# Performance work log

Hardware: AMD Instinct MI355X
Metric: run time of the kernel (lower is better)

Reference implementation:

```python
import jax, jax.numpy as jnp
import numpy as np

B, S, N, E = 8, 64, 512, 32  # batch, seq_size, node_num, embed_size


def setup_inputs() -> dict:
    key = jax.random.key(0)
    k0, k1, k2, k3, k4 = jax.random.split(key, 5)
    x = jax.random.normal(k0, (B, S, N), dtype=jnp.float32)
    # lin_w: Linear(2*S, E) -> weight (E, 2*S), bias (E,)
    W = jax.random.normal(k1, (E, 2 * S), dtype=jnp.float32) * (1.0 / np.sqrt(2 * S))
    b_w = jax.random.normal(k2, (E,), dtype=jnp.float32) * 0.01
    # lin_a: Linear(E, 1) -> weight (E,), bias scalar
    Wa = jax.random.normal(k3, (E,), dtype=jnp.float32) * (1.0 / np.sqrt(E))
    b_a = jax.random.normal(k4, (), dtype=jnp.float32) * 0.01
    return {"x": x, "W": W, "b_w": b_w, "Wa": Wa, "b_a": b_a}


def reference(x, W, b_w, Wa, b_a):
    # Faithful to MP_GAT.forward in eval mode (dropout = identity).
    # Algebraic decomposition: lin_w(cat(vi, vj)) = vi @ Wi^T + vj @ Wj^T + b,
    # where W = [Wi | Wj] along the input dim -- avoids the O(N^2 * 2S) concat.
    s = W.shape[1] // 2
    v = jnp.transpose(x, (0, 2, 1))          # (B, N, S)
    Wi, Wj = W[:, :s], W[:, s:]              # (E, S) each
    ti = jnp.einsum('bns,es->bne', v, Wi)    # (B, N, E)
    tj = jnp.einsum('bns,es->bne', v, Wj)    # (B, N, E)
    pre = ti[:, :, None, :] + tj[:, None, :, :] + b_w  # (B, N, N, E)
    xw = jnp.where(pre > 0, pre, 0.2 * pre)  # LeakyReLU(0.2)
    e = jnp.einsum('bije,e->bij', xw, Wa) + b_a        # (B, N, N) = lin_a(...).squeeze
    attention = jax.nn.softmax(e, axis=2)
    h = jax.nn.sigmoid(jnp.einsum('bij,bjs->bis', attention, v))  # (B, N, S)
    return jnp.transpose(h, (0, 2, 1)), attention      # (B, S, N), (B, N, N)
```

## Files before the change

### kernel.cpp

```cpp
#include <hip/hip_runtime.h>
#include <math.h>

#define BB 8
#define SS 64
#define NN 512
#define EE 32
#define IT 16

__device__ __forceinline__ int swz(int i, int j) {
    return (((i >> 2) ^ ((j >> 3) & 3)) << 2) | (i & 3);
}

__global__ __launch_bounds__(256) void proj_kernel(
    const float* __restrict__ x, const float* __restrict__ W,
    const float* __restrict__ b_w, const float* __restrict__ Wa,
    float* __restrict__ tip, float* __restrict__ tjp,
    float* __restrict__ cip, float* __restrict__ djp)
{
    __shared__ float sW[SS][65];
    const int t = threadIdx.x;
    const int b = blockIdx.x >> 5;
    const int n0 = (blockIdx.x & 31) << 4;

#pragma unroll
    for (int r = 0; r < 4; ++r) {
        int idx = r * 1024 + t * 4;
        float4 w4 = *(const float4*)(W + idx);
        int e = idx >> 7;
        int sp = idx & 127;
        int eo = ((sp >> 6) << 5) | e;
        int s0 = sp & 63;
        sW[s0 + 0][eo] = w4.x;
        sW[s0 + 1][eo] = w4.y;
        sW[s0 + 2][eo] = w4.z;
        sW[s0 + 3][eo] = w4.w;
    }
    __syncthreads();

    const int eo = t & 63;
    const int ng = t >> 6;
    const float* xb = x + (size_t)b * SS * NN + n0 + (ng << 2);
    float a0 = 0.f, a1 = 0.f, a2 = 0.f, a3 = 0.f;
#pragma unroll 8
    for (int s = 0; s < SS; ++s) {
        float wv = sW[s][eo];
        float4 xv = *(const float4*)(xb + (size_t)s * NN);
        a0 = fmaf(wv, xv.x, a0);
        a1 = fmaf(wv, xv.y, a1);
        a2 = fmaf(wv, xv.z, a2);
        a3 = fmaf(wv, xv.w, a3);
    }
    const int e = eo & 31;
    const bool isI = eo < EE;
    float bias = isI ? b_w[e] : 0.f;
    a0 += bias; a1 += bias; a2 += bias; a3 += bias;
    float* dst = isI ? tip : tjp;
    *(float4*)(dst + ((size_t)(b * EE + e)) * NN + n0 + (ng << 2)) =
        make_float4(a0, a1, a2, a3);

    float wa = Wa[e];
    float r0 = wa * a0, r1 = wa * a1, r2 = wa * a2, r3 = wa * a3;
#pragma unroll
    for (int off = 1; off <= 16; off <<= 1) {
        r0 += __shfl_xor(r0, off);
        r1 += __shfl_xor(r1, off);
        r2 += __shfl_xor(r2, off);
        r3 += __shfl_xor(r3, off);
    }
    if (eo == 0)
        *(float4*)(cip + (size_t)b * NN + n0 + (ng << 2)) = make_float4(r0, r1, r2, r3);
    if (eo == 32)
        *(float4*)(djp + (size_t)b * NN + n0 + (ng << 2)) = make_float4(r0, r1, r2, r3);
}

__global__ __launch_bounds__(512, 2) void attn_kernel(
    const float* __restrict__ x,
    const float* __restrict__ tip,
    const float* __restrict__ tjp,
    const float* __restrict__ cip,
    const float* __restrict__ djp,
    const float* __restrict__ Wa,
    float* __restrict__ out0,
    float* __restrict__ out1)
{
    __shared__ float s_tiT[IT][36];
    __shared__ float scT[NN][20];
    __shared__ float red1[8][17];
    __shared__ float s_M[IT];
    __shared__ float s_inv[IT];
    __shared__ __align__(16) float ubuf[EE * NN];

    float (*stj)[NN] = (float (*)[NN])ubuf;

    const int t = threadIdx.x;
    const int b = blockIdx.x >> 5;
    const int i0 = (blockIdx.x & 31) << 4;

    {
        int e = t >> 4, ii = t & 15;
        s_tiT[ii][e] = tip[((size_t)(b * EE + e)) * NN + i0 + ii];
    }
    {
        const float4* src = (const float4*)(tjp + (size_t)b * EE * NN);
        float4* dst4 = (float4*)ubuf;
#pragma unroll
        for (int r = 0; r < 8; ++r) dst4[r * 512 + t] = src[r * 512 + t];
    }
    __syncthreads();

    const int ip = t & 7;
    const int jc = t >> 3;
    const int jb0 = jc << 3;
    const int ia = 2 * ip, ibb = 2 * ip + 1;

    float rti0[EE], rti1[EE];
#pragma unroll
    for (int q = 0; q < 8; ++q) {
        float4 v = *(const float4*)(&s_tiT[ia][q << 2]);
        rti0[4 * q + 0] = v.x; rti0[4 * q + 1] = v.y;
        rti0[4 * q + 2] = v.z; rti0[4 * q + 3] = v.w;
        float4 w = *(const float4*)(&s_tiT[ibb][q << 2]);
        rti1[4 * q + 0] = w.x; rti1[4 * q + 1] = w.y;
        rti1[4 * q + 2] = w.z; rti1[4 * q + 3] = w.w;
    }

    float acc0[8], acc1[8];
#pragma unroll
    for (int k = 0; k < 8; ++k) { acc0[k] = 0.f; acc1[k] = 0.f; }

#pragma unroll
    for (int e = 0; e < EE; ++e) {
        float wa = Wa[e];
        float t0 = rti0[e], t1 = rti1[e];
        float4 ja = *(const float4*)(&stj[e][jb0]);
        float4 jb = *(const float4*)(&stj[e][jb0 + 4]);
        float tj8[8] = {ja.x, ja.y, ja.z, ja.w, jb.x, jb.y, jb.z, jb.w};
#pragma unroll
        for (int k = 0; k < 8; ++k) {
            float p0 = fmaxf(t0 + tj8[k], 0.f);
            acc0[k] = fmaf(p0, wa, acc0[k]);
            float p1 = fmaxf(t1 + tj8[k], 0.f);
            acc1[k] = fmaf(p1, wa, acc1[k]);
        }
    }

    float dj8[8];
    {
        float4 d0 = *(const float4*)(djp + (size_t)b * NN + jb0);
        float4 d1 = *(const float4*)(djp + (size_t)b * NN + jb0 + 4);
        dj8[0] = d0.x; dj8[1] = d0.y; dj8[2] = d0.z; dj8[3] = d0.w;
        dj8[4] = d1.x; dj8[5] = d1.y; dj8[6] = d1.z; dj8[7] = d1.w;
    }
    float c0 = 0.2f * cip[(size_t)b * NN + i0 + ia];
    float c1 = 0.2f * cip[(size_t)b * NN + i0 + ibb];
    float sc0[8], sc1[8];
#pragma unroll
    for (int k = 0; k < 8; ++k) {
        sc0[k] = fmaf(0.8f, acc0[k], fmaf(0.2f, dj8[k], c0));
        sc1[k] = fmaf(0.8f, acc1[k], fmaf(0.2f, dj8[k], c1));
    }

    float m0 = sc0[0], m1 = sc1[0];
#pragma unroll
    for (int k = 1; k < 8; ++k) { m0 = fmaxf(m0, sc0[k]); m1 = fmaxf(m1, sc1[k]); }
#pragma unroll
    for (int off = 8; off <= 32; off <<= 1) {
        m0 = fmaxf(m0, __shfl_xor(m0, off));
        m1 = fmaxf(m1, __shfl_xor(m1, off));
    }
    const int wv = t >> 6;
    if ((t & 56) == 0) { red1[wv][ia] = m0; red1[wv][ibb] = m1; }
    __syncthreads();
    if (t < IT) {
        float M = red1[0][t];
#pragma unroll
        for (int g = 1; g < 8; ++g) M = fmaxf(M, red1[g][t]);
        s_M[t] = M;
    }
    __syncthreads();

    float M0 = s_M[ia], M1 = s_M[ibb];
    float pr0[8], pr1[8];
#pragma unroll
    for (int k = 0; k < 8; ++k) {
        pr0[k] = __expf(sc0[k] - M0);
        pr1[k] = __expf(sc1[k] - M1);
    }
#pragma unroll
    for (int k = 0; k < 8; ++k) {
        int j = jb0 + k;
        scT[j][swz(ia, j)] = pr0[k];
        scT[j][swz(ibb, j)] = pr1[k];
    }
    float q0 = 0.f, q1 = 0.f;
#pragma unroll
    for (int k = 0; k < 8; ++k) { q0 += pr0[k]; q1 += pr1[k]; }
#pragma unroll
    for (int off = 8; off <= 32; off <<= 1) {
        q0 += __shfl_xor(q0, off);
        q1 += __shfl_xor(q1, off);
    }
    if ((t & 56) == 0) { red1[wv][ia] = q0; red1[wv][ibb] = q1; }
    __syncthreads();
    if (t < IT) {
        float S = 0.f;
#pragma unroll
        for (int g = 0; g < 8; ++g) S += red1[g][t];
        s_inv[t] = 1.0f / S;
    }
    __syncthreads();

    {
        float v0 = s_inv[ia], v1 = s_inv[ibb];
        float* r0p = out1 + ((size_t)(b * NN + i0 + ia)) * NN + jb0;
        float* r1p = out1 + ((size_t)(b * NN + i0 + ibb)) * NN + jb0;
        *(float4*)(r0p)     = make_float4(pr0[0]*v0, pr0[1]*v0, pr0[2]*v0, pr0[3]*v0);
        *(float4*)(r0p + 4) = make_float4(pr0[4]*v0, pr0[5]*v0, pr0[6]*v0, pr0[7]*v0);
        *(float4*)(r1p)     = make_float4(pr1[0]*v1, pr1[1]*v1, pr1[2]*v1, pr1[3]*v1);
        *(float4*)(r1p + 4) = make_float4(pr1[4]*v1, pr1[5]*v1, pr1[6]*v1, pr1[7]*v1);
    }

    const int jw = t & 3, sq = (t >> 2) & 7, ih = (t >> 5) & 1, w8 = t >> 6;
    float pacc[8][8];
#pragma unroll
    for (int r = 0; r < 8; ++r)
#pragma unroll
        for (int c = 0; c < 8; ++c) pacc[r][c] = 0.f;

    const float* xbb = x + (size_t)b * SS * NN;
#pragma unroll
    for (int uu = 0; uu < 4; ++uu) {
        const int jb = uu * 128 + w8 * 16 + jw * 4;
        float xq[8][4];
#pragma unroll
        for (int r = 0; r < 8; ++r) {
            float4 xv = *(const float4*)(xbb + (size_t)(sq + 8 * r) * NN + jb);
            xq[r][0] = xv.x; xq[r][1] = xv.y; xq[r][2] = xv.z; xq[r][3] = xv.w;
        }
#pragma unroll
        for (int v = 0; v < 4; ++v) {
            int j2 = jb + v;
            int key = (j2 >> 3) & 3;
            float4 pA4 = *(const float4*)(&scT[j2][((2 * ih) ^ key) << 2]);
            float4 pB4 = *(const float4*)(&scT[j2][((2 * ih + 1) ^ key) << 2]);
            float pA[4] = {pA4.x, pA4.y, pA4.z, pA4.w};
            float pB[4] = {pB4.x, pB4.y, pB4.z, pB4.w};
#pragma unroll
            for (int r = 0; r < 8; ++r) {
                float xv = xq[r][v];
#pragma unroll
                for (int c = 0; c < 4; ++c) {
                    pacc[r][c]     = fmaf(xv, pA[c], pacc[r][c]);
                    pacc[r][4 + c] = fmaf(xv, pB[c], pacc[r][4 + c]);
                }
            }
        }
    }

#pragma unroll
    for (int r = 0; r < 8; ++r)
#pragma unroll
        for (int c = 0; c < 8; ++c) {
            float v = pacc[r][c];
            v += __int_as_float(__builtin_amdgcn_mov_dpp(__float_as_int(v), 0xB1, 0xF, 0xF, true));
            v += __int_as_float(__builtin_amdgcn_mov_dpp(__float_as_int(v), 0x4E, 0xF, 0xF, true));
            pacc[r][c] = v;
        }
    if (jw == 0) {
#pragma unroll
        for (int r = 0; r < 8; ++r) {
            int s = sq + 8 * r;
            float* hq = &ubuf[(size_t)(w8 * SS + s) * 20 + ih * 8];
            *(float4*)(hq)     = make_float4(pacc[r][0], pacc[r][1], pacc[r][2], pacc[r][3]);
            *(float4*)(hq + 4) = make_float4(pacc[r][4], pacc[r][5], pacc[r][6], pacc[r][7]);
        }
    }
    __syncthreads();

    {
        int i = t & 15, sp = t >> 4;
        float vi = s_inv[i];
#pragma unroll
        for (int p = 0; p < 2; ++p) {
            int s = sp + 32 * p;
            float h = 0.f;
#pragma unroll
            for (int wq = 0; wq < 8; ++wq) h += ubuf[(size_t)(wq * SS + s) * 20 + i];
            h *= vi;
            out0[((size_t)(b * SS + s)) * NN + i0 + i] = 1.0f / (1.0f + __expf(-h));
        }
    }
}

extern "C" void kernel_launch(void* const* d_in, const int* in_sizes, int n_in,
                              void* d_out, int out_size, void* d_ws, size_t ws_size,
                              hipStream_t stream) {
    const float* x   = (const float*)d_in[0];
    const float* W   = (const float*)d_in[1];
    const float* b_w = (const float*)d_in[2];
    const float* Wa  = (const float*)d_in[3];

    float* out0 = (float*)d_out;
    float* out1 = (float*)d_out + (size_t)BB * SS * NN;

    float* tip = (float*)d_ws;
    float* tjp = tip + (size_t)BB * EE * NN;
    float* cip = tjp + (size_t)BB * EE * NN;
    float* djp = cip + (size_t)BB * NN;

    proj_kernel<<<BB * (NN / 16), 256, 0, stream>>>(x, W, b_w, Wa, tip, tjp, cip, djp);
    attn_kernel<<<BB * (NN / IT), 512, 0, stream>>>(x, tip, tjp, cip, djp, Wa, out0, out1);
}
```

Measured before the change: 23.59 us.

## Store tj and softmax probabilities as bf16, drop max pass, use abs LeakyReLU form

The tj projection is written to the workspace as packed bf16, halving the global and shared traffic for the tj tile in the attention kernel. Unnormalized probabilities are also kept in LDS as packed bf16, and the PV loop unpacks eight values from a single 16-byte read. LeakyReLU is rewritten as 0.6x + 0.4|x|, which folds the linear part into the precomputed ci/dj terms. The softmax max-reduction pass and its two barriers are removed, and block indices are remapped across XCDs with a smaller proj block. The risks are bf16 rounding error in the attention weights and exp overflow when scores are large, since the max is no longer subtracted.

After: 22.22 us. 5.8% less time.

```diff
diff --git a/kernel.cpp b/kernel.cpp
--- a/kernel.cpp
+++ b/kernel.cpp
@@ -7,24 +7,35 @@
 #define EE 32
 #define IT 16
 
-__device__ __forceinline__ int swz(int i, int j) {
-    return (((i >> 2) ^ ((j >> 3) & 3)) << 2) | (i & 3);
-}
-
-__global__ __launch_bounds__(256) void proj_kernel(
+__device__ __forceinline__ unsigned short f2bf(float f) {
+    union { float f; unsigned u; } v; v.f = f;
+    unsigned r = v.u + 0x7fffu + ((v.u >> 16) & 1u);
+    return (unsigned short)(r >> 16);
+}
+__device__ __forceinline__ float bflo(unsigned u) { return __uint_as_float(u << 16); }
+__device__ __forceinline__ float bfhi(unsigned u) { return __uint_as_float(u & 0xffff0000u); }
+
+__device__ __forceinline__ float qsum(float v) {
+    v += __int_as_float(__builtin_amdgcn_mov_dpp(__float_as_int(v), 0xB1, 0xF, 0xF, true));
+    v += __int_as_float(__builtin_amdgcn_mov_dpp(__float_as_int(v), 0x4E, 0xF, 0xF, true));
+    return v;
+}
+
+__global__ __launch_bounds__(128) void proj_kernel(
     const float* __restrict__ x, const float* __restrict__ W,
     const float* __restrict__ b_w, const float* __restrict__ Wa,
-    float* __restrict__ tip, float* __restrict__ tjp,
+    float* __restrict__ tip, unsigned short* __restrict__ tjb,
     float* __restrict__ cip, float* __restrict__ djp)
 {
     __shared__ float sW[SS][65];
     const int t = threadIdx.x;
-    const int b = blockIdx.x >> 5;
-    const int n0 = (blockIdx.x & 31) << 4;
-
-#pragma unroll
-    for (int r = 0; r < 4; ++r) {
-        int idx = r * 1024 + t * 4;
+    const int wg = ((blockIdx.x & 7) << 6) | (blockIdx.x >> 3);
+    const int b = wg >> 6;
+    const int n0 = (wg & 63) << 3;
+
+#pragma unroll
+    for (int r = 0; r < 8; ++r) {
+        int idx = r * 512 + t * 4;
         float4 w4 = *(const float4*)(W + idx);
         int e = idx >> 7;
         int sp = idx & 127;
@@ -52,11 +63,17 @@
     }
     const int e = eo & 31;
     const bool isI = eo < EE;
-    float bias = isI ? b_w[e] : 0.f;
-    a0 += bias; a1 += bias; a2 += bias; a3 += bias;
-    float* dst = isI ? tip : tjp;
-    *(float4*)(dst + ((size_t)(b * EE + e)) * NN + n0 + (ng << 2)) =
-        make_float4(a0, a1, a2, a3);
+    if (isI) {
+        float bias = b_w[e];
+        a0 += bias; a1 += bias; a2 += bias; a3 += bias;
+        *(float4*)(tip + ((size_t)(b * EE + e)) * NN + n0 + (ng << 2)) =
+            make_float4(a0, a1, a2, a3);
+    } else {
+        unsigned u0 = f2bf(a0) | ((unsigned)f2bf(a1) << 16);
+        unsigned u1 = f2bf(a2) | ((unsigned)f2bf(a3) << 16);
+        *(uint2*)(tjb + ((size_t)(b * EE + e)) * NN + n0 + (ng << 2)) =
+            make_uint2(u0, u1);
+    }
 
     float wa = Wa[e];
     float r0 = wa * a0, r1 = wa * a1, r2 = wa * a2, r3 = wa * a3;
@@ -76,52 +93,53 @@
 __global__ __launch_bounds__(512, 2) void attn_kernel(
     const float* __restrict__ x,
     const float* __restrict__ tip,
-    const float* __restrict__ tjp,
+    const unsigned short* __restrict__ tjb,
     const float* __restrict__ cip,
     const float* __restrict__ djp,
     const float* __restrict__ Wa,
     float* __restrict__ out0,
     float* __restrict__ out1)
 {
-    __shared__ float s_tiT[IT][36];
-    __shared__ float scT[NN][20];
-    __shared__ float red1[8][17];
-    __shared__ float s_M[IT];
+    __shared__ __align__(16) unsigned short stj[EE * NN];
+    __shared__ __align__(16) unsigned scT[NN * 12];
+    __shared__ __align__(16) float s_tiT[IT][36];
+    __shared__ __align__(16) float hp[8 * SS * 20];
+    __shared__ __align__(16) float red[8][IT];
     __shared__ float s_inv[IT];
-    __shared__ __align__(16) float ubuf[EE * NN];
-
-    float (*stj)[NN] = (float (*)[NN])ubuf;
 
     const int t = threadIdx.x;
-    const int b = blockIdx.x >> 5;
-    const int i0 = (blockIdx.x & 31) << 4;
-
-    {
-        int e = t >> 4, ii = t & 15;
-        s_tiT[ii][e] = tip[((size_t)(b * EE + e)) * NN + i0 + ii];
-    }
-    {
-        const float4* src = (const float4*)(tjp + (size_t)b * EE * NN);
-        float4* dst4 = (float4*)ubuf;
-#pragma unroll
-        for (int r = 0; r < 8; ++r) dst4[r * 512 + t] = src[r * 512 + t];
+    const int wg = ((blockIdx.x & 7) << 5) | (blockIdx.x >> 3);
+    const int b = wg >> 5;
+    const int i0 = (wg & 31) << 4;
+    const int lane = t & 63;
+    const int w = t >> 6;
+
+    {
+        int i = t & 15, e = t >> 4;
+        s_tiT[i][e] = tip[((size_t)(b * EE + e)) * NN + i0 + i];
+    }
+    {
+        const uint4* src = (const uint4*)(tjb + (size_t)b * EE * NN);
+        uint4* dst = (uint4*)stj;
+#pragma unroll
+        for (int r = 0; r < 4; ++r) dst[r * 512 + t] = src[r * 512 + t];
     }
     __syncthreads();
 
     const int ip = t & 7;
     const int jc = t >> 3;
-    const int jb0 = jc << 3;
-    const int ia = 2 * ip, ibb = 2 * ip + 1;
+    const int j0 = jc << 3;
+    const int ia = 2 * ip, ib2 = 2 * ip + 1;
 
     float rti0[EE], rti1[EE];
 #pragma unroll
     for (int q = 0; q < 8; ++q) {
-        float4 v = *(const float4*)(&s_tiT[ia][q << 2]);
+        float4 v = *(const float4*)&s_tiT[ia][q << 2];
         rti0[4 * q + 0] = v.x; rti0[4 * q + 1] = v.y;
         rti0[4 * q + 2] = v.z; rti0[4 * q + 3] = v.w;
-        float4 w = *(const float4*)(&s_tiT[ibb][q << 2]);
-        rti1[4 * q + 0] = w.x; rti1[4 * q + 1] = w.y;
-        rti1[4 * q + 2] = w.z; rti1[4 * q + 3] = w.w;
+        float4 u = *(const float4*)&s_tiT[ib2][q << 2];
+        rti1[4 * q + 0] = u.x; rti1[4 * q + 1] = u.y;
+        rti1[4 * q + 2] = u.z; rti1[4 * q + 3] = u.w;
     }
 
     float acc0[8], acc1[8];
@@ -130,97 +148,74 @@
 
 #pragma unroll
     for (int e = 0; e < EE; ++e) {
+        uint4 d = *(const uint4*)&stj[e * NN + j0];
         float wa = Wa[e];
         float t0 = rti0[e], t1 = rti1[e];
-        float4 ja = *(const float4*)(&stj[e][jb0]);
-        float4 jb = *(const float4*)(&stj[e][jb0 + 4]);
-        float tj8[8] = {ja.x, ja.y, ja.z, ja.w, jb.x, jb.y, jb.z, jb.w};
+        float tjf[8];
+        tjf[0] = bflo(d.x); tjf[1] = bfhi(d.x);
+        tjf[2] = bflo(d.y); tjf[3] = bfhi(d.y);
+        tjf[4] = bflo(d.z); tjf[5] = bfhi(d.z);
+        tjf[6] = bflo(d.w); tjf[7] = bfhi(d.w);
 #pragma unroll
         for (int k = 0; k < 8; ++k) {
-            float p0 = fmaxf(t0 + tj8[k], 0.f);
-            acc0[k] = fmaf(p0, wa, acc0[k]);
-            float p1 = fmaxf(t1 + tj8[k], 0.f);
-            acc1[k] = fmaf(p1, wa, acc1[k]);
+            acc0[k] = fmaf(fabsf(t0 + tjf[k]), wa, acc0[k]);
+            acc1[k] = fmaf(fabsf(t1 + tjf[k]), wa, acc1[k]);
         }
     }
 
     float dj8[8];
     {
-        float4 d0 = *(const float4*)(djp + (size_t)b * NN + jb0);
-        float4 d1 = *(const float4*)(djp + (size_t)b * NN + jb0 + 4);
+        float4 d0 = *(const float4*)(djp + (size_t)b * NN + j0);
+        float4 d1 = *(const float4*)(djp + (size_t)b * NN + j0 + 4);
         dj8[0] = d0.x; dj8[1] = d0.y; dj8[2] = d0.z; dj8[3] = d0.w;
         dj8[4] = d1.x; dj8[5] = d1.y; dj8[6] = d1.z; dj8[7] = d1.w;
     }
-    float c0 = 0.2f * cip[(size_t)b * NN + i0 + ia];
-    float c1 = 0.2f * cip[(size_t)b * NN + i0 + ibb];
-    float sc0[8], sc1[8];
+    float c0 = cip[(size_t)b * NN + i0 + ia];
+    float c1 = cip[(size_t)b * NN + i0 + ib2];
+    float pr0[8], pr1[8];
 #pragma unroll
     for (int k = 0; k < 8; ++k) {
-        sc0[k] = fmaf(0.8f, acc0[k], fmaf(0.2f, dj8[k], c0));
-        sc1[k] = fmaf(0.8f, acc1[k], fmaf(0.2f, dj8[k], c1));
-    }
-
-    float m0 = sc0[0], m1 = sc1[0];
-#pragma unroll
-    for (int k = 1; k < 8; ++k) { m0 = fmaxf(m0, sc0[k]); m1 = fmaxf(m1, sc1[k]); }
+        pr0[k] = __expf(fmaf(0.4f, acc0[k], 0.6f * (c0 + dj8[k])));
+        pr1[k] = __expf(fmaf(0.4f, acc1[k], 0.6f * (c1 + dj8[k])));
+    }
+
+#pragma unroll
+    for (int k = 0; k < 8; ++k) {
+        scT[(j0 + k) * 12 + ip] = f2bf(pr0[k]) | ((unsigned)f2bf(pr1[k]) << 16);
+    }
+
+    float rs0 = 0.f, rs1 = 0.f;
+#pragma unroll
+    for (int k = 0; k < 8; ++k) { rs0 += pr0[k]; rs1 += pr1[k]; }
 #pragma unroll
     for (int off = 8; off <= 32; off <<= 1) {
-        m0 = fmaxf(m0, __shfl_xor(m0, off));
-        m1 = fmaxf(m1, __shfl_xor(m1, off));
-    }
-    const int wv = t >> 6;
-    if ((t & 56) == 0) { red1[wv][ia] = m0; red1[wv][ibb] = m1; }
-    __syncthreads();
-    if (t < IT) {
-        float M = red1[0][t];
-#pragma unroll
-        for (int g = 1; g < 8; ++g) M = fmaxf(M, red1[g][t]);
-        s_M[t] = M;
-    }
-    __syncthreads();
-
-    float M0 = s_M[ia], M1 = s_M[ibb];
-    float pr0[8], pr1[8];
-#pragma unroll
-    for (int k = 0; k < 8; ++k) {
-        pr0[k] = __expf(sc0[k] - M0);
-        pr1[k] = __expf(sc1[k] - M1);
-    }
-#pragma unroll
-    for (int k = 0; k < 8; ++k) {
-        int j = jb0 + k;
-        scT[j][swz(ia, j)] = pr0[k];
-        scT[j][swz(ibb, j)] = pr1[k];
-    }
-    float q0 = 0.f, q1 = 0.f;
-#pragma unroll
-    for (int k = 0; k < 8; ++k) { q0 += pr0[k]; q1 += pr1[k]; }
-#pragma unroll
-    for (int off = 8; off <= 32; off <<= 1) {
-        q0 += __shfl_xor(q0, off);
-        q1 += __shfl_xor(q1, off);
-    }
-    if ((t & 56) == 0) { red1[wv][ia] = q0; red1[wv][ibb] = q1; }
+        rs0 += __shfl_xor(rs0, off);
+        rs1 += __shfl_xor(rs1, off);
+    }
+    if (lane < 8) { red[w][2 * lane] = rs0; red[w][2 * lane + 1] = rs1; }
     __syncthreads();
     if (t < IT) {
         float S = 0.f;
 #pragma unroll
-        for (int g = 0; g < 8; ++g) S += red1[g][t];
+        for (int ww = 0; ww < 8; ++ww) S += red[ww][t];
         s_inv[t] = 1.0f / S;
     }
     __syncthreads();
 
     {
-        float v0 = s_inv[ia], v1 = s_inv[ibb];
-        float* r0p = out1 + ((size_t)(b * NN + i0 + ia)) * NN + jb0;
-        float* r1p = out1 + ((size_t)(b * NN + i0 + ibb)) * NN + jb0;
+        float v0 = s_inv[ia], v1 = s_inv[ib2];
+        float* r0p = out1 + ((size_t)(b * NN + i0 + ia)) * NN + j0;
+        float* r1p = out1 + ((size_t)(b * NN + i0 + ib2)) * NN + j0;
         *(float4*)(r0p)     = make_float4(pr0[0]*v0, pr0[1]*v0, pr0[2]*v0, pr0[3]*v0);
         *(float4*)(r0p + 4) = make_float4(pr0[4]*v0, pr0[5]*v0, pr0[6]*v0, pr0[7]*v0);
         *(float4*)(r1p)     = make_float4(pr1[0]*v1, pr1[1]*v1, pr1[2]*v1, pr1[3]*v1);
         *(float4*)(r1p + 4) = make_float4(pr1[4]*v1, pr1[5]*v1, pr1[6]*v1, pr1[7]*v1);
     }
 
-    const int jw = t & 3, sq = (t >> 2) & 7, ih = (t >> 5) & 1, w8 = t >> 6;
+    const int jw = t & 3;
+    const int sq = (t >> 2) & 7;
+    const int ih = (t >> 5) & 1;
+    const int w8 = t >> 6;
     float pacc[8][8];
 #pragma unroll
     for (int r = 0; r < 8; ++r)
@@ -239,20 +234,18 @@
         }
 #pragma unroll
         for (int v = 0; v < 4; ++v) {
-            int j2 = jb + v;
-            int key = (j2 >> 3) & 3;
-            float4 pA4 = *(const float4*)(&scT[j2][((2 * ih) ^ key) << 2]);
-            float4 pB4 = *(const float4*)(&scT[j2][((2 * ih + 1) ^ key) << 2]);
-            float pA[4] = {pA4.x, pA4.y, pA4.z, pA4.w};
-            float pB[4] = {pB4.x, pB4.y, pB4.z, pB4.w};
+            uint4 dd = *(const uint4*)&scT[(jb + v) * 12 + (ih << 2)];
+            float ps[8];
+            ps[0] = bflo(dd.x); ps[1] = bfhi(dd.x);
+            ps[2] = bflo(dd.y); ps[3] = bfhi(dd.y);
+            ps[4] = bflo(dd.z); ps[5] = bfhi(dd.z);
+            ps[6] = bflo(dd.w); ps[7] = bfhi(dd.w);
 #pragma unroll
             for (int r = 0; r < 8; ++r) {
                 float xv = xq[r][v];
 #pragma unroll
-                for (int c = 0; c < 4; ++c) {
-                    pacc[r][c]     = fmaf(xv, pA[c], pacc[r][c]);
-                    pacc[r][4 + c] = fmaf(xv, pB[c], pacc[r][4 + c]);
-                }
+                for (int c = 0; c < 8; ++c)
+                    pacc[r][c] = fmaf(xv, ps[c], pacc[r][c]);
             }
         }
     }
@@ -260,17 +253,13 @@
 #pragma unroll
     for (int r = 0; r < 8; ++r)
 #pragma unroll
-        for (int c = 0; c < 8; ++c) {
-            float v = pacc[r][c];
-            v += __int_as_float(__builtin_amdgcn_mov_dpp(__float_as_int(v), 0xB1, 0xF, 0xF, true));
-            v += __int_as_float(__builtin_amdgcn_mov_dpp(__float_as_int(v), 0x4E, 0xF, 0xF, true));
-            pacc[r][c] = v;
-        }
+        for (int c = 0; c < 8; ++c) pacc[r][c] = qsum(pacc[r][c]);
+
     if (jw == 0) {
 #pragma unroll
         for (int r = 0; r < 8; ++r) {
             int s = sq + 8 * r;
-            float* hq = &ubuf[(size_t)(w8 * SS + s) * 20 + ih * 8];
+            float* hq = &hp[(w8 * SS + s) * 20 + ih * 8];
             *(float4*)(hq)     = make_float4(pacc[r][0], pacc[r][1], pacc[r][2], pacc[r][3]);
             *(float4*)(hq + 4) = make_float4(pacc[r][4], pacc[r][5], pacc[r][6], pacc[r][7]);
         }
@@ -278,14 +267,14 @@
     __syncthreads();
 
     {
-        int i = t & 15, sp = t >> 4;
+        int i = t & 15, sb = t >> 4;
         float vi = s_inv[i];
 #pragma unroll
-        for (int p = 0; p < 2; ++p) {
-            int s = sp + 32 * p;
+        for (int rr = 0; rr < 2; ++rr) {
+            int s = sb + 32 * rr;
             float h = 0.f;
 #pragma unroll
-            for (int wq = 0; wq < 8; ++wq) h += ubuf[(size_t)(wq * SS + s) * 20 + i];
+            for (int ww = 0; ww < 8; ++ww) h += hp[(ww * SS + s) * 20 + i];
             h *= vi;
             out0[((size_t)(b * SS + s)) * NN + i0 + i] = 1.0f / (1.0f + __expf(-h));
         }
@@ -304,10 +293,10 @@
     float* out1 = (float*)d_out + (size_t)BB * SS * NN;
 
     float* tip = (float*)d_ws;
-    float* tjp = tip + (size_t)BB * EE * NN;
-    float* cip = tjp + (size_t)BB * EE * NN;
+    unsigned short* tjb = (unsigned short*)(tip + (size_t)BB * EE * NN);
+    float* cip = (float*)(tjb + (size_t)BB * EE * NN);
     float* djp = cip + (size_t)BB * NN;
 
-    proj_kernel<<<BB * (NN / 16), 256, 0, stream>>>(x, W, b_w, Wa, tip, tjp, cip, djp);
-    attn_kernel<<<BB * (NN / IT), 512, 0, stream>>>(x, tip, tjp, cip, djp, Wa, out0, out1);
-}
+    proj_kernel<<<BB * (NN / 8), 128, 0, stream>>>(x, W, b_w, Wa, tip, tjb, cip, djp);
+    attn_kernel<<<BB * (NN / IT), 512, 0, stream>>>(x, tip, tjb, cip, djp, Wa, out0, out1);
+}
```
